# Optimization experiments

Hardware: AMD Instinct MI355X
Metric: run time of the kernel (lower is better)

Reference implementation:

```python
import jax, jax.numpy as jnp
import numpy as np

B, N, C = 8, 2048, 3
E, H, NB, K = 256, 8, 3, 32
OUT_PTS = N // 2
EPS = 1e-5


def _ln(x, g, b):
    mu = jnp.mean(x, -1, keepdims=True)
    v = jnp.var(x, -1, keepdims=True)
    return g * (x - mu) / jnp.sqrt(v + EPS) + b


def _bn(x, g, b, axes):
    # train-mode BatchNorm1d: per-feature batch stats (biased variance)
    mu = jnp.mean(x, axes, keepdims=True)
    v = jnp.var(x, axes, keepdims=True)
    return g * (x - mu) / jnp.sqrt(v + EPS) + b


def setup_inputs() -> dict:
    key = jax.random.key(0)
    ks = jax.random.split(key, 20)
    rn = lambda k, shape, s: jax.random.normal(k, shape, jnp.float32) * s
    inp = {}
    inp['x'] = jax.random.normal(ks[0], (B, N, C), jnp.float32)
    # ARPE params
    inp['W1'] = rn(ks[1], (2 * C, 2 * C), 0.3)
    inp['b1'] = jnp.zeros((2 * C,), jnp.float32)
    inp['g1'] = jnp.ones((2 * C,), jnp.float32)
    inp['be1'] = jnp.zeros((2 * C,), jnp.float32)
    inp['W2'] = rn(ks[2], (2 * C, E), 0.3)
    inp['b2'] = jnp.zeros((E,), jnp.float32)
    inp['g2'] = jnp.ones((E,), jnp.float32)
    inp['be2'] = jnp.zeros((E,), jnp.float32)
    # transformer block params (stacked over NB blocks)
    inp['ln1_g'] = jnp.ones((NB, E), jnp.float32)
    inp['ln1_b'] = jnp.zeros((NB, E), jnp.float32)
    inp['attn_w'] = rn(ks[3], (NB, E, 3 * E), 0.02)
    inp['attn_b'] = jnp.zeros((NB, 3 * E), jnp.float32)
    inp['out_w'] = rn(ks[4], (NB, E, E), 0.02)
    inp['out_b'] = jnp.zeros((NB, E), jnp.float32)
    inp['ln2_g'] = jnp.ones((NB, E), jnp.float32)
    inp['ln2_b'] = jnp.zeros((NB, E), jnp.float32)
    inp['ff1_w'] = rn(ks[5], (NB, E, 2 * E), 0.02)
    inp['ff1_b'] = jnp.zeros((NB, 2 * E), jnp.float32)
    inp['ff2_w'] = rn(ks[6], (NB, 2 * E, E), 0.02)
    inp['ff2_b'] = jnp.zeros((NB, E), jnp.float32)
    # decoder params
    inp['dec1_w'] = rn(ks[7], (E, 2 * E), 0.02)
    inp['dec1_b'] = jnp.zeros((2 * E,), jnp.float32)
    inp['dec2_w'] = rn(ks[8], (2 * E, OUT_PTS * 3), 0.02)
    inp['dec2_b'] = jnp.zeros((OUT_PTS * 3,), jnp.float32)
    return inp


def _forward(x, W1, b1, g1, be1, W2, b2, g2, be2,
             ln1_g, ln1_b, attn_w, attn_b, out_w, out_b,
             ln2_g, ln2_b, ff1_w, ff1_b, ff2_w, ff2_b,
             dec1_w, dec1_b, dec2_w, dec2_b):
    Bv, Nv, Cv = x.shape
    # --- ARPE: KNN gather + diff-concat + MLP/BN/ELU + max-pool ---
    sq = jnp.sum(x * x, -1)  # [B,N]
    d2 = sq[:, :, None] + sq[:, None, :] - 2.0 * jnp.einsum('bnc,bmc->bnm', x, x)
    idx = jax.lax.top_k(-d2, K)[1]  # [B,N,K] nearest (incl. self)
    knn = jax.vmap(lambda pts, i: pts[i])(x, idx)  # [B,N,K,C]
    diffs = x[:, :, None, :] - knn
    feat = jnp.concatenate([jnp.broadcast_to(x[:, :, None, :], diffs.shape), diffs], -1)  # [B,N,K,2C]
    h = feat @ W1 + b1
    h = jax.nn.elu(_bn(h, g1, be1, (0, 1, 2)))
    h = jnp.max(h, axis=2)  # max-pool over K -> [B,N,2C]
    h = h @ W2 + b2
    h = jax.nn.elu(_bn(h, g2, be2, (0, 1)))  # [B,N,E]
    # --- transformer blocks (pre-LN; residual adds the LN'd x, per source) ---
    dh = E // H
    scale = 1.0 / np.sqrt(dh)
    xcur = h
    for i in range(NB):
        hn = _ln(xcur, ln1_g[i], ln1_b[i])
        qkv = hn @ attn_w[i] + attn_b[i]
        q, k_, v = jnp.split(qkv, 3, axis=-1)
        q = q.reshape(Bv, Nv, H, dh)
        k_ = k_.reshape(Bv, Nv, H, dh)
        v = v.reshape(Bv, Nv, H, dh)
        att = jax.nn.softmax(jnp.einsum('bnhd,bmhd->bhnm', q, k_) * scale, axis=-1)
        o = jnp.einsum('bhnm,bmhd->bnhd', att, v).reshape(Bv, Nv, E)
        xcur = o @ out_w[i] + out_b[i] + hn
        hn2 = _ln(xcur, ln2_g[i], ln2_b[i])
        ff = jax.nn.gelu(hn2 @ ff1_w[i] + ff1_b[i], approximate=False) @ ff2_w[i] + ff2_b[i]
        xcur = ff + xcur
    # --- decoder ---
    m = jnp.mean(xcur, axis=1)  # [B,E]
    d = jax.nn.gelu(m @ dec1_w + dec1_b, approximate=False) @ dec2_w + dec2_b
    return d.reshape(Bv, OUT_PTS, 3)


def reference(x, W1, b1, g1, be1, W2, b2, g2, be2,
              ln1_g, ln1_b, attn_w, attn_b, out_w, out_b,
              ln2_g, ln2_b, ff1_w, ff1_b, ff2_w, ff2_b,
              dec1_w, dec1_b, dec2_w, dec2_b):
    return _forward(x, W1, b1, g1, be1, W2, b2, g2, be2,
                    ln1_g, ln1_b, attn_w, attn_b, out_w, out_b,
                    ln2_g, ln2_b, ff1_w, ff1_b, ff2_w, ff2_b,
                    dec1_w, dec1_b, dec2_w, dec2_b)
```

## Files before the change

### kernel.cpp

```cpp
#include <hip/hip_runtime.h>
#include <math.h>
#include <float.h>

#define Bb 8
#define Nn 2048
#define Ee 256
#define Hh 8
#define NB 3
#define KK 32
#define DH 32
#define QKV 768
#define FF 512
#define OUTPTS 1024

#define CEXP 0.25509667991878083f

typedef __bf16 bf16x8 __attribute__((ext_vector_type(8)));
typedef __bf16 bf16x4 __attribute__((ext_vector_type(4)));
typedef float f32x4 __attribute__((ext_vector_type(4)));
typedef float f32x16 __attribute__((ext_vector_type(16)));
typedef unsigned u32x2 __attribute__((ext_vector_type(2)));

#if __has_builtin(__builtin_amdgcn_exp2f)
#define EXP2(x) __builtin_amdgcn_exp2f(x)
#else
#define EXP2(x) exp2f(x)
#endif

static __device__ __forceinline__ float geluf(float v) {
    return 0.5f * v * (1.0f + erff(v * 0.70710678118654752f));
}
static __device__ __forceinline__ float eluf(float v) {
    return v > 0.0f ? v : expm1f(v);
}
static __device__ __forceinline__ unsigned pkbf(float a, float b) {
    union { __bf16 h[2]; unsigned u; } t;
    t.h[0] = (__bf16)a; t.h[1] = (__bf16)b;
    return t.u;
}
static __device__ __forceinline__ void swap32(unsigned a, unsigned b, unsigned& outA, unsigned& outB, int hi) {
#if __has_builtin(__builtin_amdgcn_permlane32_swap)
    u32x2 r = __builtin_amdgcn_permlane32_swap(a, b, false, false);
    outA = r[0]; outB = r[1];
#else
    unsigned ax = (unsigned)__shfl_xor((int)a, 32, 64);
    unsigned bx = (unsigned)__shfl_xor((int)b, 32, 64);
    outB = hi ? ax : b;
    outA = hi ? a : bx;
#endif
}

#if __has_builtin(__builtin_amdgcn_global_load_lds)
#define HAVE_GLOAD_LDS 1
static __device__ __forceinline__ void gl_lds16(const __bf16* g, __bf16* l) {
    __builtin_amdgcn_global_load_lds(
        (const __attribute__((address_space(1))) unsigned*)g,
        (__attribute__((address_space(3))) unsigned*)l, 16, 0, 0);
}
#else
#define HAVE_GLOAD_LDS 0
#endif

__global__ __launch_bounds__(256) void k_knn(const float* __restrict__ x,
                                             int* __restrict__ idx) {
    int q = blockIdx.x * 4 + (threadIdx.x >> 6);
    int lane = threadIdx.x & 63;
    int b = q >> 11, n = q & (Nn - 1);
    const float* xb = x + (size_t)b * Nn * 3;
    float xn0 = xb[n * 3], xn1 = xb[n * 3 + 1], xn2 = xb[n * 3 + 2];
    float sqn = xn0 * xn0 + xn1 * xn1 + xn2 * xn2;

    unsigned cand[32];
#pragma unroll
    for (int c = 0; c < 32; ++c) {
        int m = lane + 64 * c;
        float xm0 = xb[m * 3], xm1 = xb[m * 3 + 1], xm2 = xb[m * 3 + 2];
        float sqm = xm0 * xm0 + xm1 * xm1 + xm2 * xm2;
        float d = sqn + sqm - 2.0f * (xn0 * xm0 + xn1 * xm1 + xn2 * xm2);
        unsigned fb = __float_as_uint(d);
        cand[c] = (fb & 0x80000000u) ? ~fb : (fb | 0x80000000u);
    }

    unsigned prefix = 0u;
    for (int bit = 31; bit >= 0; --bit) {
        unsigned t = prefix | (1u << bit);
        int cnt = 0;
#pragma unroll
        for (int c = 0; c < 32; ++c)
            cnt += (int)__popcll(__ballot(cand[c] < t));
        if (cnt < KK) prefix = t;
    }

    unsigned long long lmask = (1ULL << lane) - 1ULL;
    int base = 0;
#pragma unroll
    for (int c = 0; c < 32; ++c) {
        bool sel = cand[c] < prefix;
        unsigned long long mk = __ballot(sel);
        int pos = base + (int)__popcll(mk & lmask);
        if (sel) idx[(size_t)q * KK + pos] = lane + 64 * c;
        base += (int)__popcll(mk);
    }
    for (int c = 0; c < 32 && base < KK; ++c) {
        bool eq = (cand[c] == prefix);
        unsigned long long mk = __ballot(eq);
        int pos = base + (int)__popcll(mk & lmask);
        if (eq && pos < KK) idx[(size_t)q * KK + pos] = lane + 64 * c;
        base += (int)__popcll(mk);
    }
}

__global__ __launch_bounds__(256) void k_h1(const float* __restrict__ x, const int* __restrict__ idx,
                                            const float* __restrict__ W1, const float* __restrict__ b1,
                                            float* __restrict__ h1) {
    int t = blockIdx.x * 256 + threadIdx.x;
    if (t >= Bb * Nn * KK) return;
    int bn = t / KK;
    int b = bn / Nn, n = bn % Nn;
    int j = idx[t];
    const float* xb = x + (size_t)b * Nn * 3;
    float xn0 = xb[n * 3], xn1 = xb[n * 3 + 1], xn2 = xb[n * 3 + 2];
    float f3 = xn0 - xb[j * 3], f4 = xn1 - xb[j * 3 + 1], f5 = xn2 - xb[j * 3 + 2];
    float* o = h1 + (size_t)t * 6;
#pragma unroll
    for (int c = 0; c < 6; ++c) {
        o[c] = b1[c] + xn0 * W1[0 * 6 + c] + xn1 * W1[1 * 6 + c] + xn2 * W1[2 * 6 + c]
             + f3 * W1[3 * 6 + c] + f4 * W1[4 * 6 + c] + f5 * W1[5 * 6 + c];
    }
}

__global__ __launch_bounds__(256) void k_stats6_part(const float* __restrict__ v, int R, int nblk,
                                                     double* __restrict__ part) {
    int blk = blockIdx.x, tid = threadIdx.x;
    int rows = R / nblk;
    int r0 = blk * rows;
    double s[6] = {0, 0, 0, 0, 0, 0}, s2[6] = {0, 0, 0, 0, 0, 0};
    for (int r = r0 + tid; r < r0 + rows; r += 256) {
        const float* p = v + (size_t)r * 6;
#pragma unroll
        for (int c = 0; c < 6; ++c) { double t = p[c]; s[c] += t; s2[c] += t * t; }
    }
    __shared__ double sh[256][12];
#pragma unroll
    for (int c = 0; c < 6; ++c) { sh[tid][c] = s[c]; sh[tid][6 + c] = s2[c]; }
    __syncthreads();
    for (int st = 128; st > 0; st >>= 1) {
        if (tid < st) {
#pragma unroll
            for (int q = 0; q < 12; ++q) sh[tid][q] += sh[tid + st][q];
        }
        __syncthreads();
    }
    if (tid < 12) part[(size_t)blk * 12 + tid] = sh[0][tid];
}

__global__ __launch_bounds__(64) void k_stats6_fin(const double* __restrict__ part, int nblk, int R,
                                                   float* __restrict__ mean, float* __restrict__ rstd) {
    int q = threadIdx.x;
    __shared__ double tot[12];
    if (q < 12) {
        double s = 0.0;
        for (int b = 0; b < nblk; ++b) s += part[(size_t)b * 12 + q];
        tot[q] = s;
    }
    __syncthreads();
    if (q < 6) {
        double mu = tot[q] / R;
        double var = tot[6 + q] / R - mu * mu;
        mean[q] = (float)mu;
        rstd[q] = (float)(1.0 / sqrt(var + 1e-5));
    }
}

__global__ __launch_bounds__(256) void k_stats256_part(const float* __restrict__ v, int R, int nblk,
                                                       double* __restrict__ part) {
    int blk = blockIdx.x, c = threadIdx.x;
    int rows = R / nblk;
    int r0 = blk * rows;
    double s = 0.0, s2 = 0.0;
    for (int r = r0; r < r0 + rows; ++r) {
        double t = v[(size_t)r * Ee + c];
        s += t; s2 += t * t;
    }
    part[(size_t)blk * (2 * Ee) + c] = s;
    part[(size_t)blk * (2 * Ee) + Ee + c] = s2;
}

__global__ __launch_bounds__(256) void k_stats256_fin(const double* __restrict__ part, int nblk, int R,
                                                      float* __restrict__ mean, float* __restrict__ rstd) {
    int c = threadIdx.x;
    double s = 0.0, s2 = 0.0;
    for (int b = 0; b < nblk; ++b) {
        s += part[(size_t)b * (2 * Ee) + c];
        s2 += part[(size_t)b * (2 * Ee) + Ee + c];
    }
    double mu = s / R;
    double var = s2 / R - mu * mu;
    mean[c] = (float)mu;
    rstd[c] = (float)(1.0 / sqrt(var + 1e-5));
}

__global__ __launch_bounds__(256) void k_maxh2(const float* __restrict__ h1,
                                               const float* __restrict__ mean1, const float* __restrict__ rstd1,
                                               const float* __restrict__ g1, const float* __restrict__ be1,
                                               const float* __restrict__ W2, const float* __restrict__ b2,
                                               float* __restrict__ x0) {
    int bn = blockIdx.x;
    int t = threadIdx.x;
    __shared__ float hval[KK][6];
    __shared__ float hmax[6];
    if (t < KK * 6) {
        int k = t / 6, c = t % 6;
        float v = h1[((size_t)bn * KK + k) * 6 + c];
        v = (v - mean1[c]) * rstd1[c] * g1[c] + be1[c];
        hval[k][c] = eluf(v);
    }
    __syncthreads();
    if (t < 6) {
        float m = -FLT_MAX;
        for (int k = 0; k < KK; ++k) m = fmaxf(m, hval[k][t]);
        hmax[t] = m;
    }
    __syncthreads();
    float s = b2[t];
#pragma unroll
    for (int i = 0; i < 6; ++i) s += hmax[i] * W2[i * Ee + t];
    x0[(size_t)bn * Ee + t] = s;
}

__global__ __launch_bounds__(256) void k_bn2apply(float* __restrict__ x0,
                                                  const float* __restrict__ mean2, const float* __restrict__ rstd2,
                                                  const float* __restrict__ g2, const float* __restrict__ be2) {
    int i = blockIdx.x * 256 + threadIdx.x;
    if (i < Bb * Nn * Ee) {
        int c = i & (Ee - 1);
        float v = (x0[i] - mean2[c]) * rstd2[c] * g2[c] + be2[c];
        x0[i] = eluf(v);
    }
}

__global__ __launch_bounds__(256) void k_lnb(const float* __restrict__ X,
                                             const float* __restrict__ g, const float* __restrict__ b,
                                             __bf16* __restrict__ Yb) {
    int row = blockIdx.x * 4 + (threadIdx.x >> 6);
    int lane = threadIdx.x & 63;
    float4 v = *(const float4*)(X + (size_t)row * Ee + lane * 4);
    float s = v.x + v.y + v.z + v.w;
#pragma unroll
    for (int off = 32; off; off >>= 1) s += __shfl_xor(s, off, 64);
    float mu = s * (1.0f / Ee);
    float d0 = v.x - mu, d1 = v.y - mu, d2 = v.z - mu, d3 = v.w - mu;
    float s2 = d0 * d0 + d1 * d1 + d2 * d2 + d3 * d3;
#pragma unroll
    for (int off = 32; off; off >>= 1) s2 += __shfl_xor(s2, off, 64);
    float rstd = 1.0f / sqrtf(s2 * (1.0f / Ee) + 1e-5f);
    float4 gv = *(const float4*)(g + lane * 4);
    float4 bv = *(const float4*)(b + lane * 4);
    bf16x4 o;
    o[0] = (__bf16)(gv.x * d0 * rstd + bv.x);
    o[1] = (__bf16)(gv.y * d1 * rstd + bv.y);
    o[2] = (__bf16)(gv.z * d2 * rstd + bv.z);
    o[3] = (__bf16)(gv.w * d3 * rstd + bv.w);
    *(bf16x4*)(Yb + (size_t)row * Ee + lane * 4) = o;
}

__global__ __launch_bounds__(256) void k_wtall(const float* __restrict__ attn_w, const float* __restrict__ out_w,
                                               const float* __restrict__ ff1_w, const float* __restrict__ ff2_w,
                                               __bf16* __restrict__ attn_wt, __bf16* __restrict__ out_wt,
                                               __bf16* __restrict__ ff1_wt, __bf16* __restrict__ ff2_wt) {
    int bid = blockIdx.x;
    const float* w; __bf16* wt; int K, N, n0, k0;
    if (bid < 144) {
        int r = bid; int z = r / 48; r %= 48;
        K = Ee; N = QKV; n0 = (r % 12) * 64; k0 = (r / 12) * 64;
        w = attn_w + (size_t)z * K * N; wt = attn_wt + (size_t)z * K * N;
    } else if (bid < 192) {
        int r = bid - 144; int z = r / 16; r %= 16;
        K = Ee; N = Ee; n0 = (r % 4) * 64; k0 = (r / 4) * 64;
        w = out_w + (size_t)z * K * N; wt = out_wt + (size_t)z * K * N;
    } else if (bid < 288) {
        int r = bid - 192; int z = r / 32; r %= 32;
        K = Ee; N = FF; n0 = (r % 8) * 64; k0 = (r / 8) * 64;
        w = ff1_w + (size_t)z * K * N; wt = ff1_wt + (size_t)z * K * N;
    } else {
        int r = bid - 288; int z = r / 32; r %= 32;
        K = FF; N = Ee; n0 = (r % 4) * 64; k0 = (r / 4) * 64;
        w = ff2_w + (size_t)z * K * N; wt = ff2_wt + (size_t)z * K * N;
    }
    __shared__ float L[64][65];
    int t = threadIdx.x;
    int r = t >> 4, c4 = (t & 15) * 4;
#pragma unroll
    for (int j = 0; j < 4; ++j) {
        float4 v = *(const float4*)(w + (size_t)(k0 + r + j * 16) * N + n0 + c4);
        L[r + j * 16][c4 + 0] = v.x; L[r + j * 16][c4 + 1] = v.y;
        L[r + j * 16][c4 + 2] = v.z; L[r + j * 16][c4 + 3] = v.w;
    }
    __syncthreads();
#pragma unroll
    for (int j = 0; j < 4; ++j) {
        int nn = r + j * 16;
        bf16x4 o;
        o[0] = (__bf16)L[c4 + 0][nn]; o[1] = (__bf16)L[c4 + 1][nn];
        o[2] = (__bf16)L[c4 + 2][nn]; o[3] = (__bf16)L[c4 + 3][nn];
        *(bf16x4*)(wt + (size_t)(n0 + nn) * K + k0 + c4) = o;
    }
}

template<int OUTM, int RESM, int ACT, int QKVM>
__global__ __launch_bounds__(256) void k_mgemm(const __bf16* __restrict__ Ain,
                                               const __bf16* __restrict__ Wt,
                                               const float* __restrict__ bias,
                                               const void* __restrict__ res,
                                               void* __restrict__ out,
                                               int Kd, int Nd) {
    __shared__ __bf16 As[64 * 32];
    __shared__ __bf16 Bs[128 * 32];
    int tid = threadIdx.x;
    int n0 = blockIdx.x * 128, m0 = blockIdx.y * 64;
    int wave = tid >> 6, lane = tid & 63;
    int wr = wave >> 1, wc = wave & 1;
    int t = lane & 15, gg = lane >> 4;
    f32x4 acc[2][4];
#pragma unroll
    for (int m = 0; m < 2; ++m)
#pragma unroll
        for (int nn = 0; nn < 4; ++nn) acc[m][nn] = (f32x4){0.f, 0.f, 0.f, 0.f};
    int r0 = tid >> 2, g0 = tid & 3;
    for (int kt = 0; kt < Kd; kt += 32) {
#if HAVE_GLOAD_LDS
        __syncthreads();
        gl_lds16(Ain + (size_t)(m0 + r0) * Kd + kt + g0 * 8, &As[r0 * 32 + g0 * 8]);
        gl_lds16(Wt + (size_t)(n0 + r0) * Kd + kt + g0 * 8, &Bs[r0 * 32 + g0 * 8]);
        gl_lds16(Wt + (size_t)(n0 + 64 + r0) * Kd + kt + g0 * 8, &Bs[(64 + r0) * 32 + g0 * 8]);
        __syncthreads();
#else
        bf16x8 a0 = *(const bf16x8*)(Ain + (size_t)(m0 + r0) * Kd + kt + g0 * 8);
        bf16x8 w0 = *(const bf16x8*)(Wt + (size_t)(n0 + r0) * Kd + kt + g0 * 8);
        bf16x8 w1 = *(const bf16x8*)(Wt + (size_t)(n0 + 64 + r0) * Kd + kt + g0 * 8);
        __syncthreads();
        *(bf16x8*)&As[r0 * 32 + g0 * 8] = a0;
        *(bf16x8*)&Bs[r0 * 32 + g0 * 8] = w0;
        *(bf16x8*)&Bs[(64 + r0) * 32 + g0 * 8] = w1;
        __syncthreads();
#endif
        bf16x8 af[2], bfr[4];
#pragma unroll
        for (int m = 0; m < 2; ++m) af[m] = *(const bf16x8*)&As[(wr * 32 + m * 16 + t) * 32 + gg * 8];
#pragma unroll
        for (int nn = 0; nn < 4; ++nn) bfr[nn] = *(const bf16x8*)&Bs[(wc * 64 + nn * 16 + t) * 32 + gg * 8];
#pragma unroll
        for (int m = 0; m < 2; ++m)
#pragma unroll
            for (int nn = 0; nn < 4; ++nn)
                acc[m][nn] = __builtin_amdgcn_mfma_f32_16x16x32_bf16(af[m], bfr[nn], acc[m][nn], 0, 0, 0);
    }
#pragma unroll
    for (int m = 0; m < 2; ++m) {
#pragma unroll
        for (int nn = 0; nn < 4; ++nn) {
            int ocol = n0 + wc * 64 + nn * 16 + t;
            float bv = bias[ocol];
#pragma unroll
            for (int j = 0; j < 4; ++j) {
                int orow = m0 + wr * 32 + m * 16 + gg * 4 + j;
                float v = acc[m][nn][j] + bv;
                if (RESM == 1) v += (float)((const __bf16*)res)[(size_t)orow * Nd + ocol];
                if (RESM == 2) v += ((const float*)res)[(size_t)orow * Nd + ocol];
                if (ACT == 1) v = geluf(v);
                if (QKVM == 1 && ocol < Ee) v *= CEXP;
                if (OUTM == 0) ((float*)out)[(size_t)orow * Nd + ocol] = v;
                else           ((__bf16*)out)[(size_t)orow * Nd + ocol] = (__bf16)v;
            }
        }
    }
}

__global__ __launch_bounds__(256) void k_attn(const __bf16* __restrict__ qkv, __bf16* __restrict__ obf) {
    int wgid = (blockIdx.x & 7) * 128 + (blockIdx.x >> 3);
    int qg = wgid & 15;
    int bh = wgid >> 4;
    int h = bh & 7, b = bh >> 3;
    int wave = threadIdx.x >> 6, lane = threadIdx.x & 63;
    int l31 = lane & 31, hi = lane >> 5;
    int qb = qg * 128 + wave * 32;
    const size_t base = (size_t)b * Nn * QKV;

    const __bf16* qrow = qkv + base + (size_t)(qb + l31) * QKV + h * DH;
    bf16x8 qf0 = *(const bf16x8*)(qrow + hi * 8);
    bf16x8 qf1 = *(const bf16x8*)(qrow + 16 + hi * 8);

    const __bf16* vbase = qkv + base + 2 * Ee + h * DH + l31;

    f32x16 oacc = {0.f,0.f,0.f,0.f,0.f,0.f,0.f,0.f,0.f,0.f,0.f,0.f,0.f,0.f,0.f,0.f};
    float lsum = 0.0f;

    for (int c0 = 0; c0 < Nn; c0 += 32) {
        const __bf16* krow = qkv + base + (size_t)(c0 + l31) * QKV + Ee + h * DH;
        bf16x8 kf0 = *(const bf16x8*)(krow + hi * 8);
        bf16x8 kf1 = *(const bf16x8*)(krow + 16 + hi * 8);

        f32x16 s = {0.f,0.f,0.f,0.f,0.f,0.f,0.f,0.f,0.f,0.f,0.f,0.f,0.f,0.f,0.f,0.f};
        s = __builtin_amdgcn_mfma_f32_32x32x16_bf16(kf0, qf0, s, 0, 0, 0);
        s = __builtin_amdgcn_mfma_f32_32x32x16_bf16(kf1, qf1, s, 0, 0, 0);

        float p[16];
#pragma unroll
        for (int i = 0; i < 16; ++i) p[i] = EXP2(s[i]);
        float s0 = (p[0] + p[1]) + (p[2] + p[3]);
        float s1 = (p[4] + p[5]) + (p[6] + p[7]);
        float s2r = (p[8] + p[9]) + (p[10] + p[11]);
        float s3 = (p[12] + p[13]) + (p[14] + p[15]);
        lsum += (s0 + s1) + (s2r + s3);

        unsigned d0 = pkbf(p[0], p[1]),  d1 = pkbf(p[2], p[3]);
        unsigned d2 = pkbf(p[4], p[5]),  d3 = pkbf(p[6], p[7]);
        unsigned d4 = pkbf(p[8], p[9]),  d5 = pkbf(p[10], p[11]);
        unsigned d6 = pkbf(p[12], p[13]), d7 = pkbf(p[14], p[15]);
        unsigned w0a, w0b, w1a, w1b, w2a, w2b, w3a, w3b;
        swap32(d2, d0, w2a, w0a, hi);
        swap32(d3, d1, w3a, w1a, hi);
        swap32(d6, d4, w2b, w0b, hi);
        swap32(d7, d5, w3b, w1b, hi);
        union { unsigned u[4]; bf16x8 v; } pa0, pa1;
        pa0.u[0] = w0a; pa0.u[1] = w1a; pa0.u[2] = w2a; pa0.u[3] = w3a;
        pa1.u[0] = w0b; pa1.u[1] = w1b; pa1.u[2] = w2b; pa1.u[3] = w3b;

        union { __bf16 hh[8]; bf16x8 v; } vf0, vf1;
        const __bf16* vp = vbase + (size_t)(c0 + hi * 8) * QKV;
#pragma unroll
        for (int j = 0; j < 8; ++j) vf0.hh[j] = vp[(size_t)j * QKV];
#pragma unroll
        for (int j = 0; j < 8; ++j) vf1.hh[j] = vp[(size_t)(16 + j) * QKV];

        oacc = __builtin_amdgcn_mfma_f32_32x32x16_bf16(pa0.v, vf0.v, oacc, 0, 0, 0);
        oacc = __builtin_amdgcn_mfma_f32_32x32x16_bf16(pa1.v, vf1.v, oacc, 0, 0, 0);
    }

    float ltot = lsum + __shfl_xor(lsum, 32, 64);
    float invl = 1.0f / ltot;
#pragma unroll
    for (int reg = 0; reg < 16; ++reg) {
        int row = (reg & 3) + 8 * (reg >> 2) + 4 * hi;
        float iv = __shfl(invl, row, 64);
        obf[((size_t)(b * Nn + qb + row)) * Ee + h * DH + l31] = (__bf16)(oacc[reg] * iv);
    }
}

__global__ __launch_bounds__(256) void k_meanpart(const float* __restrict__ X, float* __restrict__ pm) {
    int chunk = blockIdx.x, b = blockIdx.y;
    int e = threadIdx.x;
    float s = 0.0f;
    for (int n = chunk * 256; n < chunk * 256 + 256; ++n)
        s += X[((size_t)b * Nn + n) * Ee + e];
    pm[(size_t)(b * 8 + chunk) * Ee + e] = s;
}
__global__ __launch_bounds__(256) void k_meanfin(const float* __restrict__ pm, float* __restrict__ m) {
    int i = blockIdx.x * 256 + threadIdx.x;
    int b = i >> 8, e = i & 255;
    float s = 0.0f;
    for (int c = 0; c < 8; ++c) s += pm[(size_t)(b * 8 + c) * Ee + e];
    m[i] = s * (1.0f / Nn);
}
__global__ __launch_bounds__(512) void k_dec1(const float* __restrict__ m, const float* __restrict__ w,
                                              const float* __restrict__ bias, float* __restrict__ t1) {
    int b = blockIdx.x, j = threadIdx.x;
    float s = bias[j];
    for (int i = 0; i < Ee; ++i) s += m[b * Ee + i] * w[i * FF + j];
    t1[b * FF + j] = geluf(s);
}
__global__ __launch_bounds__(256) void k_dec2(const float* __restrict__ t1, const float* __restrict__ w,
                                              const float* __restrict__ bias, float* __restrict__ out) {
    int i = blockIdx.x * 256 + threadIdx.x;
    int b = i / 3072, j = i % 3072;
    float s = bias[j];
    for (int k = 0; k < FF; ++k) s += t1[b * FF + k] * w[k * 3072 + j];
    out[i] = s;
}

extern "C" void kernel_launch(void* const* d_in, const int* in_sizes, int n_in,
                              void* d_out, int out_size, void* d_ws, size_t ws_size,
                              hipStream_t stream) {
    const float* x      = (const float*)d_in[0];
    const float* W1     = (const float*)d_in[1];
    const float* b1     = (const float*)d_in[2];
    const float* g1     = (const float*)d_in[3];
    const float* be1    = (const float*)d_in[4];
    const float* W2     = (const float*)d_in[5];
    const float* b2     = (const float*)d_in[6];
    const float* g2     = (const float*)d_in[7];
    const float* be2    = (const float*)d_in[8];
    const float* ln1_g  = (const float*)d_in[9];
    const float* ln1_b  = (const float*)d_in[10];
    const float* attn_w = (const float*)d_in[11];
    const float* attn_b = (const float*)d_in[12];
    const float* out_w  = (const float*)d_in[13];
    const float* out_b  = (const float*)d_in[14];
    const float* ln2_g  = (const float*)d_in[15];
    const float* ln2_b  = (const float*)d_in[16];
    const float* ff1_w  = (const float*)d_in[17];
    const float* ff1_b  = (const float*)d_in[18];
    const float* ff2_w  = (const float*)d_in[19];
    const float* ff2_b  = (const float*)d_in[20];
    const float* dec1_w = (const float*)d_in[21];
    const float* dec1_b = (const float*)d_in[22];
    const float* dec2_w = (const float*)d_in[23];
    const float* dec2_b = (const float*)d_in[24];
    (void)in_sizes; (void)n_in; (void)out_size; (void)ws_size;

    const size_t MN = (size_t)Bb * Nn * Ee;

    float*  A    = (float*)d_ws;
    __bf16* Ab   = (__bf16*)(A + MN);
    __bf16* qkvb = Ab + MN;
    __bf16* obf  = qkvb + (size_t)Bb * Nn * QKV;
    __bf16* ffb  = obf + MN;
    __bf16* attn_wt = ffb + (size_t)Bb * Nn * FF;
    __bf16* out_wt  = attn_wt + (size_t)NB * QKV * Ee;
    __bf16* ff1_wt  = out_wt + (size_t)NB * Ee * Ee;
    __bf16* ff2_wt  = ff1_wt + (size_t)NB * FF * Ee;
    float*  S       = (float*)(ff2_wt + (size_t)NB * Ee * FF);

    float* mean1 = S,      *rstd1 = S + 16;
    float* mean2 = S + 32, *rstd2 = S + 32 + Ee;
    float* pm    = S + 1024;
    float* mvec  = pm + 64 * Ee;
    float* t1    = mvec + Bb * Ee;
    double* part6   = (double*)(S + 32768);
    double* part256 = part6 + 512 * 12;

    int*   idx = (int*)qkvb;
    float* h1  = (float*)(idx + (size_t)Bb * Nn * KK);

    k_wtall<<<384, 256, 0, stream>>>(attn_w, out_w, ff1_w, ff2_w,
                                     attn_wt, out_wt, ff1_wt, ff2_wt);

    k_knn <<<Bb * Nn / 4, 256, 0, stream>>>(x, idx);
    k_h1  <<<(Bb * Nn * KK) / 256, 256, 0, stream>>>(x, idx, W1, b1, h1);
    k_stats6_part<<<512, 256, 0, stream>>>(h1, Bb * Nn * KK, 512, part6);
    k_stats6_fin<<<1, 64, 0, stream>>>(part6, 512, Bb * Nn * KK, mean1, rstd1);
    k_maxh2<<<Bb * Nn, 256, 0, stream>>>(h1, mean1, rstd1, g1, be1, W2, b2, A);
    k_stats256_part<<<64, 256, 0, stream>>>(A, Bb * Nn, 64, part256);
    k_stats256_fin<<<1, 256, 0, stream>>>(part256, 64, Bb * Nn, mean2, rstd2);
    k_bn2apply<<<(Bb * Nn * Ee) / 256, 256, 0, stream>>>(A, mean2, rstd2, g2, be2);

    const int M = Bb * Nn;
    for (int i = 0; i < NB; ++i) {
        k_lnb<<<M / 4, 256, 0, stream>>>(A, ln1_g + i * Ee, ln1_b + i * Ee, Ab);
        k_mgemm<1, 0, 0, 1><<<dim3(QKV / 128, M / 64), 256, 0, stream>>>(
            Ab, attn_wt + (size_t)i * QKV * Ee, attn_b + i * QKV, nullptr, qkvb, Ee, QKV);
        k_attn<<<Bb * Hh * 16, 256, 0, stream>>>(qkvb, obf);
        k_mgemm<0, 1, 0, 0><<<dim3(Ee / 128, M / 64), 256, 0, stream>>>(
            obf, out_wt + (size_t)i * Ee * Ee, out_b + i * Ee, Ab, A, Ee, Ee);
        k_lnb<<<M / 4, 256, 0, stream>>>(A, ln2_g + i * Ee, ln2_b + i * Ee, Ab);
        k_mgemm<1, 0, 1, 0><<<dim3(FF / 128, M / 64), 256, 0, stream>>>(
            Ab, ff1_wt + (size_t)i * FF * Ee, ff1_b + i * FF, nullptr, ffb, Ee, FF);
        k_mgemm<0, 2, 0, 0><<<dim3(Ee / 128, M / 64), 256, 0, stream>>>(
            ffb, ff2_wt + (size_t)i * Ee * FF, ff2_b + i * Ee, A, A, FF, Ee);
    }

    k_meanpart<<<dim3(8, Bb), 256, 0, stream>>>(A, pm);
    k_meanfin<<<Bb, 256, 0, stream>>>(pm, mvec);
    k_dec1<<<Bb, FF, 0, stream>>>(mvec, dec1_w, dec1_b, t1);
    k_dec2<<<(Bb * OUTPTS * 3) / 256, 256, 0, stream>>>(t1, dec2_w, dec2_b, (float*)d_out);
}
```

Baseline: 868.5 us.

## Write transposed V tiles from QKV GEMM epilogue for vectorized attention loads

The QKV GEMM epilogue now also writes the V columns into a separate buffer laid out per (batch, head, 32-key chunk, dim, key), reusing the FF scratch space. The attention kernel then reads V fragments as two 16-byte vector loads instead of sixteen strided scalar bf16 loads per iteration. This removes uncoalesced strided gathers from the attention inner loop. In exchange the GEMM epilogue does extra scattered 8-byte stores and the FF buffer is reused as scratch.

```diff
diff --git a/kernel.cpp b/kernel.cpp
--- a/kernel.cpp
+++ b/kernel.cpp
@@ -313,7 +313,8 @@
                                                const float* __restrict__ bias,
                                                const void* __restrict__ res,
                                                void* __restrict__ out,
-                                               int Kd, int Nd) {
+                                               int Kd, int Nd,
+                                               __bf16* __restrict__ vt) {
     __shared__ __bf16 As[64 * 32];
     __shared__ __bf16 Bs[128 * 32];
     int tid = threadIdx.x;
@@ -361,6 +362,7 @@
         for (int nn = 0; nn < 4; ++nn) {
             int ocol = n0 + wc * 64 + nn * 16 + t;
             float bv = bias[ocol];
+            float vv[4];
 #pragma unroll
             for (int j = 0; j < 4; ++j) {
                 int orow = m0 + wr * 32 + m * 16 + gg * 4 + j;
@@ -369,14 +371,28 @@
                 if (RESM == 2) v += ((const float*)res)[(size_t)orow * Nd + ocol];
                 if (ACT == 1) v = geluf(v);
                 if (QKVM == 1 && ocol < Ee) v *= CEXP;
+                vv[j] = v;
                 if (OUTM == 0) ((float*)out)[(size_t)orow * Nd + ocol] = v;
                 else           ((__bf16*)out)[(size_t)orow * Nd + ocol] = (__bf16)v;
             }
+            if (QKVM == 1 && ocol >= 2 * Ee) {
+                int d = ocol - 2 * Ee;
+                int h = d >> 5, dd = d & 31;
+                int orow0 = m0 + wr * 32 + m * 16 + gg * 4;
+                int bi = orow0 >> 11, n = orow0 & (Nn - 1);
+                int kc = n >> 5, k5 = n & 31;
+                bf16x4 o;
+                o[0] = (__bf16)vv[0]; o[1] = (__bf16)vv[1];
+                o[2] = (__bf16)vv[2]; o[3] = (__bf16)vv[3];
+                *(bf16x4*)(vt + ((((size_t)(bi * Hh + h) * (Nn / 32) + kc) * DH + dd) << 5) + k5) = o;
+            }
         }
     }
 }
 
-__global__ __launch_bounds__(256) void k_attn(const __bf16* __restrict__ qkv, __bf16* __restrict__ obf) {
+__global__ __launch_bounds__(256) void k_attn(const __bf16* __restrict__ qkv,
+                                              const __bf16* __restrict__ vt,
+                                              __bf16* __restrict__ obf) {
     int wgid = (blockIdx.x & 7) * 128 + (blockIdx.x >> 3);
     int qg = wgid & 15;
     int bh = wgid >> 4;
@@ -390,7 +406,7 @@
     bf16x8 qf0 = *(const bf16x8*)(qrow + hi * 8);
     bf16x8 qf1 = *(const bf16x8*)(qrow + 16 + hi * 8);
 
-    const __bf16* vbase = qkv + base + 2 * Ee + h * DH + l31;
+    const __bf16* vtb = vt + ((size_t)(b * Hh + h) * (Nn / 32)) * DH * 32 + l31 * 32 + hi * 8;
 
     f32x16 oacc = {0.f,0.f,0.f,0.f,0.f,0.f,0.f,0.f,0.f,0.f,0.f,0.f,0.f,0.f,0.f,0.f};
     float lsum = 0.0f;
@@ -426,15 +442,12 @@
         pa0.u[0] = w0a; pa0.u[1] = w1a; pa0.u[2] = w2a; pa0.u[3] = w3a;
         pa1.u[0] = w0b; pa1.u[1] = w1b; pa1.u[2] = w2b; pa1.u[3] = w3b;
 
-        union { __bf16 hh[8]; bf16x8 v; } vf0, vf1;
-        const __bf16* vp = vbase + (size_t)(c0 + hi * 8) * QKV;
-#pragma unroll
-        for (int j = 0; j < 8; ++j) vf0.hh[j] = vp[(size_t)j * QKV];
-#pragma unroll
-        for (int j = 0; j < 8; ++j) vf1.hh[j] = vp[(size_t)(16 + j) * QKV];
-
-        oacc = __builtin_amdgcn_mfma_f32_32x32x16_bf16(pa0.v, vf0.v, oacc, 0, 0, 0);
-        oacc = __builtin_amdgcn_mfma_f32_32x32x16_bf16(pa1.v, vf1.v, oacc, 0, 0, 0);
+        const __bf16* vp = vtb + (size_t)(c0 >> 5) * (DH * 32);
+        bf16x8 vf0 = *(const bf16x8*)vp;
+        bf16x8 vf1 = *(const bf16x8*)(vp + 16);
+
+        oacc = __builtin_amdgcn_mfma_f32_32x32x16_bf16(pa0.v, vf0, oacc, 0, 0, 0);
+        oacc = __builtin_amdgcn_mfma_f32_32x32x16_bf16(pa1.v, vf1, oacc, 0, 0, 0);
     }
 
     float ltot = lsum + __shfl_xor(lsum, 32, 64);
@@ -521,6 +534,8 @@
     __bf16* ff2_wt  = ff1_wt + (size_t)NB * FF * Ee;
     float*  S       = (float*)(ff2_wt + (size_t)NB * Ee * FF);
 
+    __bf16* Vt = ffb;
+
     float* mean1 = S,      *rstd1 = S + 16;
     float* mean2 = S + 32, *rstd2 = S + 32 + Ee;
     float* pm    = S + 1024;
@@ -548,15 +563,15 @@
     for (int i = 0; i < NB; ++i) {
         k_lnb<<<M / 4, 256, 0, stream>>>(A, ln1_g + i * Ee, ln1_b + i * Ee, Ab);
         k_mgemm<1, 0, 0, 1><<<dim3(QKV / 128, M / 64), 256, 0, stream>>>(
-            Ab, attn_wt + (size_t)i * QKV * Ee, attn_b + i * QKV, nullptr, qkvb, Ee, QKV);
-        k_attn<<<Bb * Hh * 16, 256, 0, stream>>>(qkvb, obf);
+            Ab, attn_wt + (size_t)i * QKV * Ee, attn_b + i * QKV, nullptr, qkvb, Ee, QKV, Vt);
+        k_attn<<<Bb * Hh * 16, 256, 0, stream>>>(qkvb, Vt, obf);
         k_mgemm<0, 1, 0, 0><<<dim3(Ee / 128, M / 64), 256, 0, stream>>>(
-            obf, out_wt + (size_t)i * Ee * Ee, out_b + i * Ee, Ab, A, Ee, Ee);
+            obf, out_wt + (size_t)i * Ee * Ee, out_b + i * Ee, Ab, A, Ee, Ee, nullptr);
         k_lnb<<<M / 4, 256, 0, stream>>>(A, ln2_g + i * Ee, ln2_b + i * Ee, Ab);
         k_mgemm<1, 0, 1, 0><<<dim3(FF / 128, M / 64), 256, 0, stream>>>(
-            Ab, ff1_wt + (size_t)i * FF * Ee, ff1_b + i * FF, nullptr, ffb, Ee, FF);
+            Ab, ff1_wt + (size_t)i * FF * Ee, ff1_b + i * FF, nullptr, ffb, Ee, FF, nullptr);
         k_mgemm<0, 2, 0, 0><<<dim3(Ee / 128, M / 64), 256, 0, stream>>>(
-            ffb, ff2_wt + (size_t)i * Ee * FF, ff2_b + i * Ee, A, A, FF, Ee);
+            ffb, ff2_wt + (size_t)i * Ee * FF, ff2_b + i * Ee, A, A, FF, Ee, nullptr);
     }
 
     k_meanpart<<<dim3(8, Bb), 256, 0, stream>>>(A, pm);
```

Measured after the change: 861.6 us. About the same (-0.8%).
